# Performance work log

Hardware: AMD Instinct MI355X
Metric: run time of the kernel (lower is better)

## Reference

```python
import jax, jax.numpy as jnp
import numpy as np

IN_FEATURES = 5
OUT_FEATURES = 10
BITS = 2
N_TOKENS = 4_000_000


def fake_quant_weight(w, bits):
    # Symmetric per-output-channel quantization.
    # levels: qmin = -2^(b-1), qmax = 2^(b-1)-1  (for bits=2: {-2,-1,0,1})
    qmax = 2 ** (bits - 1) - 1
    qmin = -(2 ** (bits - 1))
    # per-row (per output channel) scale; avoid div-by-zero
    scale = jnp.max(jnp.abs(w), axis=1, keepdims=True) / qmax  # [out, 1]
    scale = jnp.maximum(scale, 1e-8)
    w_q = jnp.clip(jnp.round(w / scale), qmin, qmax)
    return w_q * scale  # dequantized weight, [out, in]


def setup_inputs() -> dict:
    key = jax.random.key(0)
    kx, kw, kb = jax.random.split(key, 3)
    x = jax.random.normal(kx, (N_TOKENS, IN_FEATURES), dtype=jnp.float32)
    # Kaiming-uniform-ish init like nn.Linear
    bound = 1.0 / np.sqrt(IN_FEATURES)
    weight = jax.random.uniform(kw, (OUT_FEATURES, IN_FEATURES), dtype=jnp.float32,
                                minval=-bound, maxval=bound)
    bias = jax.random.uniform(kb, (OUT_FEATURES,), dtype=jnp.float32,
                              minval=-bound, maxval=bound)
    return {"x": x, "weight": weight, "bias": bias}


def reference(x, weight, bias):
    # QuantizedLinear(5, 10, bits=2): 2-bit fake-quantized weight matmul + bias.
    w_deq = fake_quant_weight(weight, BITS)            # [out, in]
    return x @ w_deq.T + bias                          # [N, out]
```

## Files before the change

kernel.cpp:

```cpp
#include <hip/hip_runtime.h>


constexpr int IN_F  = 5;
constexpr int OUT_F = 10;
constexpr int BLOCK = 256;
constexpr int TOK   = 256;

__global__ __launch_bounds__(BLOCK) void qlinear_kernel(
    const float* __restrict__ x,
    const float* __restrict__ w,
    const float* __restrict__ bias,
    float* __restrict__ out,
    int n_tokens)
{
    __shared__ float wdq[OUT_F * IN_F];
    __shared__ float bsh[OUT_F];
    __shared__ float xs[TOK * IN_F];
    __shared__ float os[TOK * OUT_F];

    const int tid = threadIdx.x;

    if (tid < OUT_F) {
        float row[IN_F];
        float mx = 0.0f;
        #pragma unroll
        for (int j = 0; j < IN_F; ++j) {
            row[j] = w[tid * IN_F + j];
            mx = fmaxf(mx, fabsf(row[j]));
        }
        const float scale = fmaxf(mx, 1e-8f);
        #pragma unroll
        for (int j = 0; j < IN_F; ++j) {
            float q = rintf(row[j] / scale);
            q = fminf(fmaxf(q, -2.0f), 1.0f);
            wdq[tid * IN_F + j] = q * scale;
        }
        bsh[tid] = bias[tid];
    }

    const long tok0 = (long)blockIdx.x * TOK;
    const bool full = (tok0 + TOK) <= (long)n_tokens;
    const long xbase = tok0 * IN_F;
    const long obase = tok0 * OUT_F;

    if (full) {
        #pragma unroll
        for (int i = 0; i < IN_F; ++i) {
            const int k = i * BLOCK + tid;
            xs[k] = __builtin_nontemporal_load(x + xbase + k);
        }
    } else {
        const long xtotal = (long)n_tokens * IN_F;
        #pragma unroll
        for (int i = 0; i < IN_F; ++i) {
            const int k = i * BLOCK + tid;
            const long gi = xbase + k;
            xs[k] = (gi < xtotal) ? x[gi] : 0.0f;
        }
    }
    __syncthreads();

    {
        float xv[IN_F];
        #pragma unroll
        for (int j = 0; j < IN_F; ++j) xv[j] = xs[tid * IN_F + j];
        #pragma unroll
        for (int o = 0; o < OUT_F; ++o) {
            float acc = bsh[o];
            #pragma unroll
            for (int j = 0; j < IN_F; ++j)
                acc = fmaf(xv[j], wdq[o * IN_F + j], acc);
            os[tid * OUT_F + o] = acc;
        }
    }
    __syncthreads();

    if (full) {
        #pragma unroll
        for (int i = 0; i < OUT_F; ++i) {
            const int k = i * BLOCK + tid;
            __builtin_nontemporal_store(os[k], out + obase + k);
        }
    } else {
        const long ototal = (long)n_tokens * OUT_F;
        #pragma unroll
        for (int i = 0; i < OUT_F; ++i) {
            const int k = i * BLOCK + tid;
            const long gi = obase + k;
            if (gi < ototal) out[gi] = os[k];
        }
    }
}

extern "C" void kernel_launch(void* const* d_in, const int* in_sizes, int n_in,
                              void* d_out, int out_size, void* d_ws, size_t ws_size,
                              hipStream_t stream) {
    const float* x    = (const float*)d_in[0];
    const float* wgt  = (const float*)d_in[1];
    const float* bias = (const float*)d_in[2];
    float* out = (float*)d_out;

    const int n_tokens = in_sizes[0] / IN_F;
    const int blocks   = (n_tokens + TOK - 1) / TOK;

    qlinear_kernel<<<blocks, BLOCK, 0, stream>>>(x, wgt, bias, out, n_tokens);
}
```

Baseline: 212.1 us.

## Vectorize global loads/stores to float4, process two tokens per thread with swizzled LDS

Doubles tokens per block so each thread computes two tokens, and moves the global-to-LDS and LDS-to-global traffic to 16-byte vector accesses instead of scalar ones. The output staging buffer uses an XOR swizzle on float4 chunk indices to reduce LDS bank conflicts on the strided per-thread writes. Nontemporal load/store hints are dropped, and the larger shared buffers (30 KB per block) may reduce occupancy.

```diff
diff --git a/kernel.cpp b/kernel.cpp
--- a/kernel.cpp
+++ b/kernel.cpp
@@ -1,10 +1,16 @@
 #include <hip/hip_runtime.h>
 
+
+typedef float f32x4 __attribute__((ext_vector_type(4)));
 
 constexpr int IN_F  = 5;
 constexpr int OUT_F = 10;
 constexpr int BLOCK = 256;
-constexpr int TOK   = 256;
+constexpr int TOK   = 512;
+constexpr int XCH   = TOK * IN_F  / 4;
+constexpr int OCH   = TOK * OUT_F / 4;
+
+__device__ __forceinline__ int swz(int c) { return c ^ ((c >> 3) & 7); }
 
 __global__ __launch_bounds__(BLOCK) void qlinear_kernel(
     const float* __restrict__ x,
@@ -15,8 +21,8 @@
 {
     __shared__ float wdq[OUT_F * IN_F];
     __shared__ float bsh[OUT_F];
-    __shared__ float xs[TOK * IN_F];
-    __shared__ float os[TOK * OUT_F];
+    __shared__ __align__(16) float xs[TOK * IN_F];
+    __shared__ __align__(16) float os[TOK * OUT_F];
 
     const int tid = threadIdx.x;
 
@@ -40,54 +46,85 @@
 
     const long tok0 = (long)blockIdx.x * TOK;
     const bool full = (tok0 + TOK) <= (long)n_tokens;
-    const long xbase = tok0 * IN_F;
-    const long obase = tok0 * OUT_F;
+
+    f32x4* xs4 = (f32x4*)xs;
+    f32x4* os4 = (f32x4*)os;
+    const f32x4* xg4 = (const f32x4*)x + tok0 * IN_F / 4;
+    f32x4*       og4 = (f32x4*)out      + tok0 * OUT_F / 4;
 
     if (full) {
         #pragma unroll
-        for (int i = 0; i < IN_F; ++i) {
+        for (int i = 0; i < 3; ++i) {
             const int k = i * BLOCK + tid;
-            xs[k] = __builtin_nontemporal_load(x + xbase + k);
+            if (k < XCH) xs4[k] = xg4[k];
         }
     } else {
-        const long xtotal = (long)n_tokens * IN_F;
+        const long xtot = (long)n_tokens * IN_F;
         #pragma unroll
-        for (int i = 0; i < IN_F; ++i) {
+        for (int i = 0; i < 3; ++i) {
             const int k = i * BLOCK + tid;
-            const long gi = xbase + k;
-            xs[k] = (gi < xtotal) ? x[gi] : 0.0f;
+            if (k < XCH) {
+                const long gf = tok0 * IN_F + (long)k * 4;
+                f32x4 v = {0.f, 0.f, 0.f, 0.f};
+                #pragma unroll
+                for (int e = 0; e < 4; ++e)
+                    if (gf + e < xtot) v[e] = x[gf + e];
+                xs4[k] = v;
+            }
         }
     }
     __syncthreads();
 
     {
-        float xv[IN_F];
+        float xv[2 * IN_F];
         #pragma unroll
-        for (int j = 0; j < IN_F; ++j) xv[j] = xs[tid * IN_F + j];
+        for (int j = 0; j < 2 * IN_F; ++j)
+            xv[j] = xs[tid * 2 * IN_F + j];
+
+        float o20[2 * OUT_F];
         #pragma unroll
-        for (int o = 0; o < OUT_F; ++o) {
-            float acc = bsh[o];
+        for (int t = 0; t < 2; ++t) {
             #pragma unroll
-            for (int j = 0; j < IN_F; ++j)
-                acc = fmaf(xv[j], wdq[o * IN_F + j], acc);
-            os[tid * OUT_F + o] = acc;
+            for (int o = 0; o < OUT_F; ++o) {
+                float acc = bsh[o];
+                #pragma unroll
+                for (int j = 0; j < IN_F; ++j)
+                    acc = fmaf(xv[t * IN_F + j], wdq[o * IN_F + j], acc);
+                o20[t * OUT_F + o] = acc;
+            }
+        }
+        #pragma unroll
+        for (int q = 0; q < 5; ++q) {
+            f32x4 v;
+            v.x = o20[4 * q + 0];
+            v.y = o20[4 * q + 1];
+            v.z = o20[4 * q + 2];
+            v.w = o20[4 * q + 3];
+            os4[swz(tid * 5 + q)] = v;
         }
     }
     __syncthreads();
 
     if (full) {
         #pragma unroll
-        for (int i = 0; i < OUT_F; ++i) {
+        for (int i = 0; i < 5; ++i) {
             const int k = i * BLOCK + tid;
-            __builtin_nontemporal_store(os[k], out + obase + k);
+            og4[k] = os4[swz(k)];
         }
     } else {
-        const long ototal = (long)n_tokens * OUT_F;
+        const long otot = (long)n_tokens * OUT_F;
         #pragma unroll
-        for (int i = 0; i < OUT_F; ++i) {
+        for (int i = 0; i < 5; ++i) {
             const int k = i * BLOCK + tid;
-            const long gi = obase + k;
-            if (gi < ototal) out[gi] = os[k];
+            const long gf = tok0 * OUT_F + (long)k * 4;
+            const f32x4 v = os4[swz(k)];
+            if (gf + 3 < otot) {
+                og4[k] = v;
+            } else {
+                #pragma unroll
+                for (int e = 0; e < 4; ++e)
+                    if (gf + e < otot) out[gf + e] = v[e];
+            }
         }
     }
 }
```

Result: slower. 219.3 us (+3.4%).

## Persistent grid with double-buffered async LDS loads and vectorized output stores

Applied to the files above, without the earlier changes.

Replaces the one-tile-per-block launch with a persistent grid of at most 2048 blocks, each looping over tiles. Input for the next tile is staged into a second LDS buffer with global_load_lds DMA while the current tile's outputs are written, using explicit vmcnt waits and raw barriers. Output stores are widened to 16-byte nontemporal vector stores. The aim is to overlap load latency with compute and stores and to cut per-block setup overhead. The cost is more fragile hand-managed synchronization that relies on vmcnt ordering.

```diff
diff --git a/kernel.cpp b/kernel.cpp
--- a/kernel.cpp
+++ b/kernel.cpp
@@ -1,10 +1,20 @@
 #include <hip/hip_runtime.h>
 
+
+typedef float f32x4 __attribute__((ext_vector_type(4)));
 
 constexpr int IN_F  = 5;
 constexpr int OUT_F = 10;
 constexpr int BLOCK = 256;
 constexpr int TOK   = 256;
+constexpr int TDWX  = TOK * IN_F;
+constexpr int WDWX  = TDWX / 4;
+constexpr int OCH   = TOK * OUT_F / 4;
+constexpr int WOCH  = OCH / 4;
+constexpr int GRID  = 2048;
+
+typedef __attribute__((address_space(3))) void       lds_void;
+typedef __attribute__((address_space(1))) const void gbl_void;
 
 __global__ __launch_bounds__(BLOCK) void qlinear_kernel(
     const float* __restrict__ x,
@@ -15,10 +25,19 @@
 {
     __shared__ float wdq[OUT_F * IN_F];
     __shared__ float bsh[OUT_F];
-    __shared__ float xs[TOK * IN_F];
-    __shared__ float os[TOK * OUT_F];
+    __shared__ __align__(16) float xs[2][TDWX];
+    __shared__ __align__(16) float os[TOK * OUT_F];
 
-    const int tid = threadIdx.x;
+    const int tid  = threadIdx.x;
+    const int wid  = tid >> 6;
+    const int lane = tid & 63;
+
+    const long ntile = ((long)n_tokens + TOK - 1) / TOK;
+    const long xtot  = (long)n_tokens * IN_F;
+    const long otot  = (long)n_tokens * OUT_F;
+
+    long tile = blockIdx.x;
+    if (tile >= ntile) return;
 
     if (tid < OUT_F) {
         float row[IN_F];
@@ -38,57 +57,91 @@
         bsh[tid] = bias[tid];
     }
 
-    const long tok0 = (long)blockIdx.x * TOK;
-    const bool full = (tok0 + TOK) <= (long)n_tokens;
-    const long xbase = tok0 * IN_F;
-    const long obase = tok0 * OUT_F;
+    auto stageDMA = [&](long t, int b) {
+        const long g0 = t * TDWX + (long)(wid * WDWX);
+        float* dst = &xs[b][wid * WDWX];
+        #pragma unroll
+        for (int i = 0; i < 5; ++i) {
+            __builtin_amdgcn_global_load_lds(
+                (gbl_void*)(x + g0 + i * 64 + lane),
+                (lds_void*)(dst + i * 64), 4, 0, 0);
+        }
+    };
+    auto stageScalar = [&](long t, int b) {
+        const long g0 = t * TDWX + (long)(wid * WDWX);
+        float* dst = &xs[b][wid * WDWX];
+        #pragma unroll
+        for (int i = 0; i < 5; ++i) {
+            const long gi = g0 + i * 64 + lane;
+            dst[i * 64 + lane] = (gi < xtot) ? x[gi] : 0.0f;
+        }
+    };
 
-    if (full) {
-        #pragma unroll
-        for (int i = 0; i < IN_F; ++i) {
-            const int k = i * BLOCK + tid;
-            xs[k] = __builtin_nontemporal_load(x + xbase + k);
+    bool staged_dma = ((tile + 1) * (long)TOK <= (long)n_tokens);
+    if (staged_dma) stageDMA(tile, 0); else stageScalar(tile, 0);
+    int  buf   = 0;
+    bool first = true;
+
+    for (; tile < ntile; tile += GRID) {
+        const long nxt = tile + GRID;
+
+        if (first || !staged_dma) {
+            asm volatile("s_waitcnt vmcnt(0)" ::: "memory");
+        } else {
+            asm volatile("s_waitcnt vmcnt(3)" ::: "memory");
         }
-    } else {
-        const long xtotal = (long)n_tokens * IN_F;
-        #pragma unroll
-        for (int i = 0; i < IN_F; ++i) {
-            const int k = i * BLOCK + tid;
-            const long gi = xbase + k;
-            xs[k] = (gi < xtotal) ? x[gi] : 0.0f;
+        asm volatile("s_waitcnt lgkmcnt(0)" ::: "memory");
+        __builtin_amdgcn_s_barrier();
+        __builtin_amdgcn_sched_barrier(0);
+        first = false;
+
+        {
+            float xv[IN_F];
+            #pragma unroll
+            for (int j = 0; j < IN_F; ++j) xv[j] = xs[buf][tid * IN_F + j];
+            #pragma unroll
+            for (int o = 0; o < OUT_F; ++o) {
+                float acc = bsh[o];
+                #pragma unroll
+                for (int c = 0; c < IN_F; ++c)
+                    acc = fmaf(xv[c], wdq[o * IN_F + c], acc);
+                os[tid * OUT_F + o] = acc;
+            }
         }
-    }
-    __syncthreads();
+        asm volatile("s_waitcnt lgkmcnt(0)" ::: "memory");
+        __builtin_amdgcn_s_barrier();
+        __builtin_amdgcn_sched_barrier(0);
 
-    {
-        float xv[IN_F];
-        #pragma unroll
-        for (int j = 0; j < IN_F; ++j) xv[j] = xs[tid * IN_F + j];
-        #pragma unroll
-        for (int o = 0; o < OUT_F; ++o) {
-            float acc = bsh[o];
+        if (nxt < ntile) {
+            staged_dma = ((nxt + 1) * (long)TOK <= (long)n_tokens);
+            if (staged_dma) stageDMA(nxt, buf ^ 1);
+            else            stageScalar(nxt, buf ^ 1);
+        }
+
+        {
+            const long oc0 = tile * (long)OCH + (long)(wid * WOCH);
+            const f32x4* os4 = (const f32x4*)os;
+            f32x4* og4 = (f32x4*)out;
             #pragma unroll
-            for (int j = 0; j < IN_F; ++j)
-                acc = fmaf(xv[j], wdq[o * IN_F + j], acc);
-            os[tid * OUT_F + o] = acc;
+            for (int i = 0; i < 3; ++i) {
+                const int nact = (i == 2) ? 32 : 64;
+                if (lane < nact) {
+                    const int  lc = wid * WOCH + i * 64 + lane;
+                    const long gc = oc0 + i * 64 + lane;
+                    const f32x4 v = os4[lc];
+                    if ((gc + 1) * 4 <= otot) {
+                        __builtin_nontemporal_store(v, og4 + gc);
+                    } else {
+                        #pragma unroll
+                        for (int e = 0; e < 4; ++e) {
+                            const long gi = gc * 4 + e;
+                            if (gi < otot) out[gi] = v[e];
+                        }
+                    }
+                }
+            }
         }
-    }
-    __syncthreads();
-
-    if (full) {
-        #pragma unroll
-        for (int i = 0; i < OUT_F; ++i) {
-            const int k = i * BLOCK + tid;
-            __builtin_nontemporal_store(os[k], out + obase + k);
-        }
-    } else {
-        const long ototal = (long)n_tokens * OUT_F;
-        #pragma unroll
-        for (int i = 0; i < OUT_F; ++i) {
-            const int k = i * BLOCK + tid;
-            const long gi = obase + k;
-            if (gi < ototal) out[gi] = os[k];
-        }
+        buf ^= 1;
     }
 }
 
@@ -100,8 +153,9 @@
     const float* bias = (const float*)d_in[2];
     float* out = (float*)d_out;
 
-    const int n_tokens = in_sizes[0] / IN_F;
-    const int blocks   = (n_tokens + TOK - 1) / TOK;
+    const int  n_tokens = in_sizes[0] / IN_F;
+    const long ntile    = ((long)n_tokens + TOK - 1) / TOK;
+    const int  blocks   = (int)(ntile < (long)GRID ? ntile : (long)GRID);
 
     qlinear_kernel<<<blocks, BLOCK, 0, stream>>>(x, wgt, bias, out, n_tokens);
 }
```

Result: slower. 222.5 us (+4.9%).
